# Kernel tuning notes

Measured on AMD Instinct MI355X. Metric: run time of the kernel, lower is better.

## Reference

```python
import jax, jax.numpy as jnp
import numpy as np
import math

N_EMBD = 1024
N_HEAD = 16
BLOCK_SIZE = 2048
B, T = 2, 2048


def setup_inputs() -> dict:
    key = jax.random.key(0)
    ks = jax.random.split(key, 12)
    s = 0.02
    C = N_EMBD
    return {
        "x": jax.random.normal(ks[0], (B, T, C), dtype=jnp.float32),
        # LayerNorm 1
        "ln1_w": jnp.ones((C,), jnp.float32),
        "ln1_b": jnp.zeros((C,), jnp.float32),
        # attention: weights stored [in, out]
        "attn_w": jax.random.normal(ks[1], (C, 3 * C), dtype=jnp.float32) * s,
        "attn_b": jnp.zeros((3 * C,), jnp.float32),
        "proj_w": jax.random.normal(ks[2], (C, C), dtype=jnp.float32) * s,
        "proj_b": jnp.zeros((C,), jnp.float32),
        # LayerNorm 2
        "ln2_w": jnp.ones((C,), jnp.float32),
        "ln2_b": jnp.zeros((C,), jnp.float32),
        # MLP
        "fc_w": jax.random.normal(ks[3], (C, 4 * C), dtype=jnp.float32) * s,
        "fc_b": jnp.zeros((4 * C,), jnp.float32),
        "mlp_proj_w": jax.random.normal(ks[4], (4 * C, C), dtype=jnp.float32) * s,
        "mlp_proj_b": jnp.zeros((C,), jnp.float32),
    }


def _layernorm(x, w, b, eps=1e-5):
    mu = jnp.mean(x, axis=-1, keepdims=True)
    var = jnp.mean(jnp.square(x - mu), axis=-1, keepdims=True)
    return (x - mu) * jax.lax.rsqrt(var + eps) * w + b


def _attention(x, attn_w, attn_b, proj_w, proj_b):
    Bn, Tn, C = x.shape
    hs = C // N_HEAD
    qkv = x @ attn_w + attn_b                      # [B,T,3C]
    q, k, v = jnp.split(qkv, 3, axis=-1)
    # [B,H,T,hs]
    q = q.reshape(Bn, Tn, N_HEAD, hs).transpose(0, 2, 1, 3)
    k = k.reshape(Bn, Tn, N_HEAD, hs).transpose(0, 2, 1, 3)
    v = v.reshape(Bn, Tn, N_HEAD, hs).transpose(0, 2, 1, 3)
    att = jnp.einsum('bhqd,bhkd->bhqk', q, k) / math.sqrt(hs)  # [B,H,T,T]
    mask = jnp.tril(jnp.ones((Tn, Tn), dtype=bool))
    att = jnp.where(mask, att, -jnp.inf)
    att = jax.nn.softmax(att, axis=-1)
    y = jnp.einsum('bhqk,bhkd->bhqd', att, v)      # [B,H,T,hs]
    y = y.transpose(0, 2, 1, 3).reshape(Bn, Tn, C)
    return y @ proj_w + proj_b


def reference(x, ln1_w, ln1_b, attn_w, attn_b, proj_w, proj_b,
              ln2_w, ln2_b, fc_w, fc_b, mlp_proj_w, mlp_proj_b):
    x = x + _attention(_layernorm(x, ln1_w, ln1_b), attn_w, attn_b, proj_w, proj_b)
    h = _layernorm(x, ln2_w, ln2_b)
    h = jax.nn.gelu(h @ fc_w + fc_b, approximate=False)  # torch nn.GELU default = exact erf
    return x + (h @ mlp_proj_w + mlp_proj_b)
```

## Files before the change

kernel.cpp:

```cpp
#include <hip/hip_runtime.h>
#include <math.h>

typedef short s8x __attribute__((ext_vector_type(8)));
typedef float f32x4 __attribute__((ext_vector_type(4)));
typedef int   i32x2 __attribute__((ext_vector_type(2)));

__device__ __forceinline__ float bf2f(short u) {
    return __uint_as_float(((unsigned int)(unsigned short)u) << 16);
}
__device__ __forceinline__ short f2bf(float f) {
    unsigned int x = __float_as_uint(f);
    unsigned int r = (x + 0x7FFFu + ((x >> 16) & 1u)) >> 16;
    return (short)(unsigned short)r;
}

__device__ __forceinline__ void gl2lds16(const short* g, const short* l) {
    __builtin_amdgcn_global_load_lds(
        (const __attribute__((address_space(1))) void*)(unsigned long long)g,
        (__attribute__((address_space(3))) void*)(unsigned int)(unsigned long long)l,
        16, 0, 0);
}

__device__ __forceinline__ void ln_row(const float* __restrict__ xin,
                                       const float* __restrict__ w,
                                       const float* __restrict__ bb,
                                       short* __restrict__ out, int row, int lane) {
    const float4* xr = (const float4*)(xin + (long)row * 1024);
    float4 v[4];
    float s1 = 0.f, s2 = 0.f;
#pragma unroll
    for (int i = 0; i < 4; ++i) {
        v[i] = xr[lane + i * 64];
        s1 += v[i].x + v[i].y + v[i].z + v[i].w;
        s2 += v[i].x*v[i].x + v[i].y*v[i].y + v[i].z*v[i].z + v[i].w*v[i].w;
    }
#pragma unroll
    for (int off = 32; off > 0; off >>= 1) {
        s1 += __shfl_xor(s1, off, 64);
        s2 += __shfl_xor(s2, off, 64);
    }
    const float mu = s1 * (1.0f / 1024.0f);
    float var = s2 * (1.0f / 1024.0f) - mu * mu;
    var = fmaxf(var, 0.0f);
    const float rs = rsqrtf(var + 1e-5f);
    short4* orow = (short4*)(out + (long)row * 1024);
#pragma unroll
    for (int i = 0; i < 4; ++i) {
        const int ci = (lane + i * 64) * 4;
        const float4 wv = *(const float4*)(w + ci);
        const float4 bv = *(const float4*)(bb + ci);
        short4 o;
        o.x = f2bf((v[i].x - mu) * rs * wv.x + bv.x);
        o.y = f2bf((v[i].y - mu) * rs * wv.y + bv.y);
        o.z = f2bf((v[i].z - mu) * rs * wv.z + bv.z);
        o.w = f2bf((v[i].w - mu) * rs * wv.w + bv.w);
        orow[lane + i * 64] = o;
    }
}

__global__ __launch_bounds__(256) void ln_k(const float* __restrict__ xin,
                                            const float* __restrict__ w,
                                            const float* __restrict__ bb,
                                            short* __restrict__ out) {
    ln_row(xin, w, bb, out, blockIdx.x * 4 + (threadIdx.x >> 6), threadIdx.x & 63);
}

__global__ __launch_bounds__(256) void pre_k(
        const float* __restrict__ w0, const float* __restrict__ w1,
        const float* __restrict__ w2, const float* __restrict__ w3,
        short* __restrict__ o0, short* __restrict__ o1,
        short* __restrict__ o2, short* __restrict__ o3,
        const float* __restrict__ x, const float* __restrict__ ln1w,
        const float* __restrict__ ln1b, short* __restrict__ xln) {
    int bid = blockIdx.x;
    if (bid >= 12288) {
        ln_row(x, ln1w, ln1b, xln, (bid - 12288) * 4 + (threadIdx.x >> 6), threadIdx.x & 63);
        return;
    }
    const float* in; short* out; int K, N, nx;
    if (bid < 3072)      { in = w0; out = o0; K = 1024; N = 3072; nx = 96; }
    else if (bid < 4096) { bid -= 3072; in = w1; out = o1; K = 1024; N = 1024; nx = 32; }
    else if (bid < 8192) { bid -= 4096; in = w2; out = o2; K = 1024; N = 4096; nx = 128; }
    else                 { bid -= 8192; in = w3; out = o3; K = 4096; N = 1024; nx = 32; }
    const int n0 = (bid % nx) * 32, k0 = (bid / nx) * 32;
    __shared__ float tile[32][33];
    const int tx = threadIdx.x & 31, ty = threadIdx.x >> 5;
#pragma unroll
    for (int i = 0; i < 4; ++i) {
        const int k = ty + i * 8;
        tile[k][tx] = in[(long)(k0 + k) * N + n0 + tx];
    }
    __syncthreads();
#pragma unroll
    for (int i = 0; i < 4; ++i) {
        const int n = ty + i * 8;
        out[(long)(n0 + n) * K + k0 + tx] = f2bf(tile[tx][n]);
    }
}

template <int EPI, typename OutT>
__device__ __forceinline__ void epi_store(OutT* out, const float* resid, long oidx, float v) {
    if constexpr (EPI == 0) {
        out[oidx] = f2bf(v);
    } else if constexpr (EPI == 1) {
        const float u = v * (0.79788456080f + 0.03567740814f * v * v);
        v = v / (1.0f + __expf(-2.0f * u));
        out[oidx] = f2bf(v);
    } else {
        v += resid[oidx];
        out[oidx] = v;
    }
}

template <int EPI, typename OutT>
__global__ __launch_bounds__(256) void gemm_k(const short* __restrict__ A,
                                              const short* __restrict__ Bt,
                                              const float* __restrict__ bias,
                                              const float* __restrict__ resid,
                                              OutT* __restrict__ out,
                                              int M, int N, int K) {
    __shared__ __align__(16) short sA[2][128 * 32];
    __shared__ __align__(16) short sB[2][128 * 32];
    const int tid = threadIdx.x;
    const int lane = tid & 63, wave = tid >> 6;
    const int wr = (wave >> 1) * 64, wc = (wave & 1) * 64;
    const int lrow = lane & 15, quad = lane >> 4;
    const int bm = blockIdx.y * 128, bn = blockIdx.x * 128;
    const short* Ap = A + (long)(bm + (tid >> 2)) * K + (tid & 3) * 8;
    const short* Bp = Bt + (long)(bn + (tid >> 2)) * K + (tid & 3) * 8;
    const long rowstep = (long)64 * K;

    auto stage = [&](int p, int k0) {
        gl2lds16(Ap + k0,           sA[p] + tid * 8);
        gl2lds16(Ap + rowstep + k0, sA[p] + 2048 + tid * 8);
        gl2lds16(Bp + k0,           sB[p] + tid * 8);
        gl2lds16(Bp + rowstep + k0, sB[p] + 2048 + tid * 8);
    };

    f32x4 acc[4][4] = {};
    stage(0, 0);
    const int S = K >> 5;
    for (int s = 0; s < S; ++s) {
        const int p = s & 1;
        __syncthreads();
        if (s + 1 < S) stage(p ^ 1, (s + 1) << 5);
        const short* pA = sA[p];
        const short* pB = sB[p];
        s8x af[4], bfr[4];
#pragma unroll
        for (int i = 0; i < 4; ++i) af[i]  = *(const s8x*)(pA + (wr + i*16 + lrow) * 32 + quad * 8);
#pragma unroll
        for (int j = 0; j < 4; ++j) bfr[j] = *(const s8x*)(pB + (wc + j*16 + lrow) * 32 + quad * 8);
#pragma unroll
        for (int i = 0; i < 4; ++i)
#pragma unroll
            for (int j = 0; j < 4; ++j)
                acc[i][j] = __builtin_amdgcn_mfma_f32_16x16x32_bf16(af[i], bfr[j], acc[i][j], 0, 0, 0);
    }
#pragma unroll
    for (int i = 0; i < 4; ++i) {
#pragma unroll
        for (int j = 0; j < 4; ++j) {
#pragma unroll
            for (int r = 0; r < 4; ++r) {
                const int row = bm + wr + i*16 + quad*4 + r;
                const int col = bn + wc + j*16 + lrow;
                epi_store<EPI>(out, resid, (long)row * N + col, acc[i][j][r] + bias[col]);
            }
        }
    }
}

template <int EPI, typename OutT>
__global__ __launch_bounds__(256) void gemm128x64_k(const short* __restrict__ A,
                                                    const short* __restrict__ Bt,
                                                    const float* __restrict__ bias,
                                                    const float* __restrict__ resid,
                                                    OutT* __restrict__ out,
                                                    int M, int N, int K) {
    __shared__ __align__(16) short sA[2][2][128 * 32];
    __shared__ __align__(16) short sB[2][2][64 * 32];
    const int tid = threadIdx.x;
    const int lane = tid & 63, wave = tid >> 6;
    const int wr = (wave >> 1) * 64, wc = (wave & 1) * 32;
    const int lrow = lane & 15, quad = lane >> 4;
    const int bm = blockIdx.y * 128, bn = blockIdx.x * 64;
    const short* Ap = A + (long)(bm + (tid >> 2)) * K + (tid & 3) * 8;
    const short* Bp = Bt + (long)(bn + (tid >> 2)) * K + (tid & 3) * 8;
    const long rowstep = (long)64 * K;

    auto stage = [&](int p, int k0) {
#pragma unroll
        for (int hp = 0; hp < 2; ++hp) {
            gl2lds16(Ap + k0 + hp * 32,           sA[p][hp] + tid * 8);
            gl2lds16(Ap + rowstep + k0 + hp * 32, sA[p][hp] + 2048 + tid * 8);
            gl2lds16(Bp + k0 + hp * 32,           sB[p][hp] + tid * 8);
        }
    };

    f32x4 acc[4][2] = {};
    stage(0, 0);
    const int S = K >> 6;
    for (int s = 0; s < S; ++s) {
        const int p = s & 1;
        __syncthreads();
        if (s + 1 < S) stage(p ^ 1, (s + 1) << 6);
#pragma unroll
        for (int hp = 0; hp < 2; ++hp) {
            s8x af[4], bfr[2];
#pragma unroll
            for (int i = 0; i < 4; ++i) af[i]  = *(const s8x*)(sA[p][hp] + (wr + i*16 + lrow) * 32 + quad * 8);
#pragma unroll
            for (int j = 0; j < 2; ++j) bfr[j] = *(const s8x*)(sB[p][hp] + (wc + j*16 + lrow) * 32 + quad * 8);
#pragma unroll
            for (int i = 0; i < 4; ++i)
#pragma unroll
                for (int j = 0; j < 2; ++j)
                    acc[i][j] = __builtin_amdgcn_mfma_f32_16x16x32_bf16(af[i], bfr[j], acc[i][j], 0, 0, 0);
        }
    }
#pragma unroll
    for (int i = 0; i < 4; ++i) {
#pragma unroll
        for (int j = 0; j < 2; ++j) {
#pragma unroll
            for (int r = 0; r < 4; ++r) {
                const int row = bm + wr + i*16 + quad*4 + r;
                const int col = bn + wc + j*16 + lrow;
                epi_store<EPI>(out, resid, (long)row * N + col, acc[i][j][r] + bias[col]);
            }
        }
    }
}

#define ATT_CS (0.125f * 1.4426950408889634f)
#define ATT_C0 (14.426950408889634f)

#define TR16(dst, off) \
    asm volatile("ds_read_b64_tr_b16 %0, %1 offset:" off : "=v"(dst) : "v"(tva))

__global__ __launch_bounds__(256) void attn_k(const short* __restrict__ qkv,
                                              short* __restrict__ y) {
    const int bx = blockIdx.x;
    const int b = blockIdx.y >> 4, h = blockIdx.y & 15;
    const int qtA = bx, qtB = 31 - bx;
    const int tid = threadIdx.x, lane = tid & 63, wave = tid >> 6;
    const int lrow = lane & 15, quad = lane >> 4;
    const long base = (long)b * 2048 * 3072;

    __shared__ __align__(16) short sK[2][64 * 64];
    __shared__ __align__(16) short sV[2][4096];

    s8x qfA0, qfA1, qfB0, qfB1;
    {
        const short* qpA = qkv + base + (long)(qtA * 64 + wave * 16 + lrow) * 3072 + h * 64 + quad * 8;
        qfA0 = *(const s8x*)qpA; qfA1 = *(const s8x*)(qpA + 32);
        const short* qpB = qkv + base + (long)(qtB * 64 + wave * 16 + lrow) * 3072 + h * 64 + quad * 8;
        qfB0 = *(const s8x*)qpB; qfB1 = *(const s8x*)(qpB + 32);
    }
    f32x4 oA[4], oB[4];
    float lA = 0.f, lB = 0.f;
#pragma unroll
    for (int d = 0; d < 4; ++d) { oA[d] = f32x4{0.f,0.f,0.f,0.f}; oB[d] = f32x4{0.f,0.f,0.f,0.f}; }

    const int srow = tid >> 3, sg = tid & 7;
    const int sw0 = ((srow & 7) ^ (srow >> 3)) & 7;
    const int sw1 = (((srow + 32) & 7) ^ ((srow + 32) >> 3)) & 7;
    const short* kbase = qkv + base + 1024 + h * 64;
    auto issueK = [&](int p, int k0) {
        gl2lds16(kbase + (long)(k0 + srow) * 3072      + (sg ^ sw0) * 8, sK[p] + tid * 8);
        gl2lds16(kbase + (long)(k0 + srow + 32) * 3072 + (sg ^ sw1) * 8, sK[p] + 2048 + tid * 8);
    };

    const int vslot   = (tid >> 3) & 7;
    const int vkbl    = 2 * (vslot & 3) + (vslot >> 2);
    const int vklocal = vkbl * 4 + ((tid >> 1) & 3);
    const short* vsrc = qkv + base + 2048 + h * 64
                      + (long)vklocal * 3072 + wave * 16 + 8 * (tid & 1);
    auto issueV = [&](int p, int k0) {
        gl2lds16(vsrc + (long)k0 * 3072,        sV[p] + tid * 8);
        gl2lds16(vsrc + (long)(k0 + 32) * 3072, sV[p] + 2048 + tid * 8);
    };
    const unsigned trb = (unsigned)(unsigned long long)(&sV[0][0]) + (unsigned)lane * 8u;

    auto tile_step = [&](const s8x& qf0, const s8x& qf1, const s8x* kf0, const s8x* kf1,
                         const s8x (*vfr)[4], f32x4* o, float& lsum, int qt, int kt, int k0) {
        f32x4 s[4];
#pragma unroll
        for (int ct = 0; ct < 4; ++ct) {
            f32x4 t = f32x4{0.f, 0.f, 0.f, 0.f};
            t = __builtin_amdgcn_mfma_f32_16x16x32_bf16(kf0[ct], qf0, t, 0, 0, 0);
            t = __builtin_amdgcn_mfma_f32_16x16x32_bf16(kf1[ct], qf1, t, 0, 0, 0);
            s[ct] = t;
        }
        const int qrow = qt * 64 + wave * 16 + lrow;
        float pv[4][4];
        if (kt == qt) {
#pragma unroll
            for (int ct = 0; ct < 4; ++ct)
#pragma unroll
                for (int r = 0; r < 4; ++r) {
                    const int key = k0 + ct * 16 + quad * 4 + r;
                    const float pp = exp2f(fmaf(s[ct][r], ATT_CS, -ATT_C0));
                    const float pt = __uint_as_float(__float_as_uint(pp) & 0xFFFF0000u);
                    pv[ct][r] = (key > qrow) ? 0.f : pt;
                }
        } else {
#pragma unroll
            for (int ct = 0; ct < 4; ++ct)
#pragma unroll
                for (int r = 0; r < 4; ++r) {
                    const float pp = exp2f(fmaf(s[ct][r], ATT_CS, -ATT_C0));
                    pv[ct][r] = __uint_as_float(__float_as_uint(pp) & 0xFFFF0000u);
                }
        }
#pragma unroll
        for (int ct = 0; ct < 4; ++ct)
            lsum += (pv[ct][0] + pv[ct][1]) + (pv[ct][2] + pv[ct][3]);

        unsigned int w2[4][2];
#pragma unroll
        for (int ct = 0; ct < 4; ++ct)
#pragma unroll
            for (int p2 = 0; p2 < 2; ++p2)
                w2[ct][p2] = __builtin_amdgcn_perm(__float_as_uint(pv[ct][2 * p2 + 1]),
                                                   __float_as_uint(pv[ct][2 * p2]), 0x07060302u);
        s8x pa[2];
#pragma unroll
        for (int ks = 0; ks < 2; ++ks) {
            auto rAC = __builtin_amdgcn_permlane32_swap((int)w2[2 * ks][0], (int)w2[2 * ks + 1][0], false, false);
            auto rBD = __builtin_amdgcn_permlane32_swap((int)w2[2 * ks][1], (int)w2[2 * ks + 1][1], false, false);
            auto mAC = __builtin_amdgcn_permlane16_swap(rAC[0], rAC[1], false, false);
            auto mBD = __builtin_amdgcn_permlane16_swap(rBD[0], rBD[1], false, false);
            int4 f;
            f.x = mAC[0]; f.y = mBD[0]; f.z = mAC[1]; f.w = mBD[1];
            pa[ks] = *(const s8x*)&f;
        }
#pragma unroll
        for (int ks = 0; ks < 2; ++ks)
#pragma unroll
            for (int dt = 0; dt < 4; ++dt)
                o[dt] = __builtin_amdgcn_mfma_f32_16x16x32_bf16(pa[ks], vfr[ks][dt], o[dt], 0, 0, 0);
    };

    issueK(0, 0);
    issueV(0, 0);
    for (int kt = 0; kt <= qtB; ++kt) {
        const int p = kt & 1, k0 = kt * 64;
        __syncthreads();
        if (kt < qtB) { issueK(p ^ 1, k0 + 64); issueV(p ^ 1, k0 + 64); }

        s8x kf0[4], kf1[4];
#pragma unroll
        for (int ct = 0; ct < 4; ++ct) {
            const int row = ct * 16 + lrow;
            const int swr = ((row & 7) ^ (row >> 3)) & 7;
            kf0[ct] = *(const s8x*)(sK[p] + row * 64 + ((quad ^ swr) * 8));
            kf1[ct] = *(const s8x*)(sK[p] + row * 64 + (((4 + quad) ^ swr) * 8));
        }

        const unsigned tva = trb + (unsigned)(p << 13);
        i32x2 tr[16];
        TR16(tr[0],  "0");    TR16(tr[1],  "512");
        TR16(tr[2],  "1024"); TR16(tr[3],  "1536");
        TR16(tr[4],  "2048"); TR16(tr[5],  "2560");
        TR16(tr[6],  "3072"); TR16(tr[7],  "3584");
        TR16(tr[8],  "4096"); TR16(tr[9],  "4608");
        TR16(tr[10], "5120"); TR16(tr[11], "5632");
        TR16(tr[12], "6144"); TR16(tr[13], "6656");
        TR16(tr[14], "7168"); TR16(tr[15], "7680");
        asm volatile("s_waitcnt lgkmcnt(0)" ::: "memory");
        __builtin_amdgcn_sched_barrier(0);
        s8x vfr[2][4];
#pragma unroll
        for (int ks = 0; ks < 2; ++ks)
#pragma unroll
            for (int dt = 0; dt < 4; ++dt) {
                const int i2 = ks * 8 + dt * 2;
                int4 f;
                f.x = tr[i2][0]; f.y = tr[i2][1];
                f.z = tr[i2 + 1][0]; f.w = tr[i2 + 1][1];
                vfr[ks][dt] = *(const s8x*)&f;
            }

        if (kt <= qtA) tile_step(qfA0, qfA1, kf0, kf1, vfr, oA, lA, qtA, kt, k0);
        tile_step(qfB0, qfB1, kf0, kf1, vfr, oB, lB, qtB, kt, k0);
    }

    lA += __shfl_xor(lA, 16, 64); lA += __shfl_xor(lA, 32, 64);
    lB += __shfl_xor(lB, 16, 64); lB += __shfl_xor(lB, 32, 64);
    float rA[4], rB[4];
#pragma unroll
    for (int r = 0; r < 4; ++r) {
        rA[r] = 1.0f / __shfl(lA, quad * 4 + r, 64);
        rB[r] = 1.0f / __shfl(lB, quad * 4 + r, 64);
    }
#pragma unroll
    for (int dt = 0; dt < 4; ++dt) {
#pragma unroll
        for (int r = 0; r < 4; ++r) {
            const int qA = qtA * 64 + wave * 16 + quad * 4 + r;
            const int qB = qtB * 64 + wave * 16 + quad * 4 + r;
            y[((long)b * 2048 + qA) * 1024 + h * 64 + dt * 16 + lrow] = f2bf(oA[dt][r] * rA[r]);
            y[((long)b * 2048 + qB) * 1024 + h * 64 + dt * 16 + lrow] = f2bf(oB[dt][r] * rB[r]);
        }
    }
}

extern "C" void kernel_launch(void* const* d_in, const int* in_sizes, int n_in,
                              void* d_out, int out_size, void* d_ws, size_t ws_size,
                              hipStream_t stream) {
    const float* x      = (const float*)d_in[0];
    const float* ln1_w  = (const float*)d_in[1];
    const float* ln1_b  = (const float*)d_in[2];
    const float* attn_w = (const float*)d_in[3];
    const float* attn_b = (const float*)d_in[4];
    const float* proj_w = (const float*)d_in[5];
    const float* proj_b = (const float*)d_in[6];
    const float* ln2_w  = (const float*)d_in[7];
    const float* ln2_b  = (const float*)d_in[8];
    const float* fc_w   = (const float*)d_in[9];
    const float* fc_b   = (const float*)d_in[10];
    const float* mlp_w  = (const float*)d_in[11];
    const float* mlp_b  = (const float*)d_in[12];

    char* ws = (char*)d_ws;
    short* attn_wt = (short*)(ws + 0);
    short* proj_wt = (short*)(ws + 6291456L);
    short* fc_wt   = (short*)(ws + 8388608L);
    short* mlp_wt  = (short*)(ws + 16777216L);
    short* slotA   = (short*)(ws + 25165824L);
    short* slotB   = (short*)(ws + 33554432L);

    short* xln  = slotA;
    short* yb   = slotA;
    short* hb   = slotA;
    short* qkvb = slotB;
    short* hh   = slotB;
    float* x1   = (float*)d_out;
    float* outp = (float*)d_out;

    pre_k<<<13312, 256, 0, stream>>>(attn_w, proj_w, fc_w, mlp_w,
                                     attn_wt, proj_wt, fc_wt, mlp_wt,
                                     x, ln1_w, ln1_b, xln);

    gemm_k<0, short><<<dim3(24, 32), 256, 0, stream>>>(xln, attn_wt, attn_b, nullptr, qkvb, 4096, 3072, 1024);
    attn_k<<<dim3(16, 32), 256, 0, stream>>>(qkvb, yb);
    gemm128x64_k<2, float><<<dim3(16, 32), 256, 0, stream>>>(yb, proj_wt, proj_b, x, x1, 4096, 1024, 1024);
    ln_k<<<1024, 256, 0, stream>>>(x1, ln2_w, ln2_b, hb);
    gemm_k<1, short><<<dim3(32, 32), 256, 0, stream>>>(hb, fc_wt, fc_b, nullptr, hh, 4096, 4096, 1024);
    gemm128x64_k<3, float><<<dim3(16, 32), 256, 0, stream>>>(hh, mlp_wt, mlp_b, x1, outp, 4096, 1024, 4096);
}
```

Before: 331.1 us.

## Triple-buffer LDS staging in GEMM and attention with explicit vmcnt waits

Moves the GEMM and attention kernels from double to triple LDS buffering. Global-to-LDS loads are issued two tiles ahead, and the full __syncthreads is replaced by an explicit vmcnt wait plus a raw s_barrier. The goal is to hide global load latency behind more MFMA work. It costs 50% more LDS per block, which may lower occupancy, and relies on correct vmcnt counting.

```diff
diff --git a/kernel.cpp b/kernel.cpp
--- a/kernel.cpp
+++ b/kernel.cpp
@@ -20,6 +20,13 @@
         (__attribute__((address_space(3))) void*)(unsigned int)(unsigned long long)l,
         16, 0, 0);
 }
+
+__device__ __forceinline__ void block_sync() {
+    asm volatile("" ::: "memory");
+    __builtin_amdgcn_s_barrier();
+    asm volatile("" ::: "memory");
+}
+#define WAITV(n) asm volatile("s_waitcnt vmcnt(" #n ")" ::: "memory")
 
 __device__ __forceinline__ void ln_row(const float* __restrict__ xin,
                                        const float* __restrict__ w,
@@ -119,8 +126,8 @@
                                               const float* __restrict__ resid,
                                               OutT* __restrict__ out,
                                               int M, int N, int K) {
-    __shared__ __align__(16) short sA[2][128 * 32];
-    __shared__ __align__(16) short sB[2][128 * 32];
+    __shared__ __align__(16) short sA[3][128 * 32];
+    __shared__ __align__(16) short sB[3][128 * 32];
     const int tid = threadIdx.x;
     const int lane = tid & 63, wave = tid >> 6;
     const int wr = (wave >> 1) * 64, wc = (wave & 1) * 64;
@@ -130,22 +137,24 @@
     const short* Bp = Bt + (long)(bn + (tid >> 2)) * K + (tid & 3) * 8;
     const long rowstep = (long)64 * K;
 
-    auto stage = [&](int p, int k0) {
-        gl2lds16(Ap + k0,           sA[p] + tid * 8);
-        gl2lds16(Ap + rowstep + k0, sA[p] + 2048 + tid * 8);
-        gl2lds16(Bp + k0,           sB[p] + tid * 8);
-        gl2lds16(Bp + rowstep + k0, sB[p] + 2048 + tid * 8);
+    auto stage = [&](int q, int k0) {
+        gl2lds16(Ap + k0,           sA[q] + tid * 8);
+        gl2lds16(Ap + rowstep + k0, sA[q] + 2048 + tid * 8);
+        gl2lds16(Bp + k0,           sB[q] + tid * 8);
+        gl2lds16(Bp + rowstep + k0, sB[q] + 2048 + tid * 8);
     };
 
     f32x4 acc[4][4] = {};
+    const int S = K >> 5;
     stage(0, 0);
-    const int S = K >> 5;
+    stage(1, 32);
+    int cur = 0, nx2 = 2;
     for (int s = 0; s < S; ++s) {
-        const int p = s & 1;
-        __syncthreads();
-        if (s + 1 < S) stage(p ^ 1, (s + 1) << 5);
-        const short* pA = sA[p];
-        const short* pB = sB[p];
+        if (s + 1 < S) { WAITV(4); } else { WAITV(0); }
+        block_sync();
+        if (s + 2 < S) stage(nx2, (s + 2) << 5);
+        const short* pA = sA[cur];
+        const short* pB = sB[cur];
         s8x af[4], bfr[4];
 #pragma unroll
         for (int i = 0; i < 4; ++i) af[i]  = *(const s8x*)(pA + (wr + i*16 + lrow) * 32 + quad * 8);
@@ -156,6 +165,8 @@
 #pragma unroll
             for (int j = 0; j < 4; ++j)
                 acc[i][j] = __builtin_amdgcn_mfma_f32_16x16x32_bf16(af[i], bfr[j], acc[i][j], 0, 0, 0);
+        cur = (cur == 2) ? 0 : cur + 1;
+        nx2 = (nx2 == 2) ? 0 : nx2 + 1;
     }
 #pragma unroll
     for (int i = 0; i < 4; ++i) {
@@ -248,8 +259,8 @@
     const int lrow = lane & 15, quad = lane >> 4;
     const long base = (long)b * 2048 * 3072;
 
-    __shared__ __align__(16) short sK[2][64 * 64];
-    __shared__ __align__(16) short sV[2][4096];
+    __shared__ __align__(16) short sK[3][64 * 64];
+    __shared__ __align__(16) short sV[3][4096];
 
     s8x qfA0, qfA1, qfB0, qfB1;
     {
@@ -267,9 +278,9 @@
     const int sw0 = ((srow & 7) ^ (srow >> 3)) & 7;
     const int sw1 = (((srow + 32) & 7) ^ ((srow + 32) >> 3)) & 7;
     const short* kbase = qkv + base + 1024 + h * 64;
-    auto issueK = [&](int p, int k0) {
-        gl2lds16(kbase + (long)(k0 + srow) * 3072      + (sg ^ sw0) * 8, sK[p] + tid * 8);
-        gl2lds16(kbase + (long)(k0 + srow + 32) * 3072 + (sg ^ sw1) * 8, sK[p] + 2048 + tid * 8);
+    auto issueK = [&](int q, int k0) {
+        gl2lds16(kbase + (long)(k0 + srow) * 3072      + (sg ^ sw0) * 8, sK[q] + tid * 8);
+        gl2lds16(kbase + (long)(k0 + srow + 32) * 3072 + (sg ^ sw1) * 8, sK[q] + 2048 + tid * 8);
     };
 
     const int vslot   = (tid >> 3) & 7;
@@ -277,9 +288,9 @@
     const int vklocal = vkbl * 4 + ((tid >> 1) & 3);
     const short* vsrc = qkv + base + 2048 + h * 64
                       + (long)vklocal * 3072 + wave * 16 + 8 * (tid & 1);
-    auto issueV = [&](int p, int k0) {
-        gl2lds16(vsrc + (long)k0 * 3072,        sV[p] + tid * 8);
-        gl2lds16(vsrc + (long)(k0 + 32) * 3072, sV[p] + 2048 + tid * 8);
+    auto issueV = [&](int q, int k0) {
+        gl2lds16(vsrc + (long)k0 * 3072,        sV[q] + tid * 8);
+        gl2lds16(vsrc + (long)(k0 + 32) * 3072, sV[q] + 2048 + tid * 8);
     };
     const unsigned trb = (unsigned)(unsigned long long)(&sV[0][0]) + (unsigned)lane * 8u;
 
@@ -343,23 +354,25 @@
                 o[dt] = __builtin_amdgcn_mfma_f32_16x16x32_bf16(pa[ks], vfr[ks][dt], o[dt], 0, 0, 0);
     };
 
-    issueK(0, 0);
-    issueV(0, 0);
+    issueK(0, 0);   issueV(0, 0);
+    issueK(1, 64);  issueV(1, 64);
+    int cur = 0, nx2 = 2;
     for (int kt = 0; kt <= qtB; ++kt) {
-        const int p = kt & 1, k0 = kt * 64;
-        __syncthreads();
-        if (kt < qtB) { issueK(p ^ 1, k0 + 64); issueV(p ^ 1, k0 + 64); }
+        const int k0 = kt * 64;
+        if (kt < qtB) { WAITV(4); } else { WAITV(0); }
+        block_sync();
+        if (kt + 2 <= qtB) { issueK(nx2, k0 + 128); issueV(nx2, k0 + 128); }
 
         s8x kf0[4], kf1[4];
 #pragma unroll
         for (int ct = 0; ct < 4; ++ct) {
             const int row = ct * 16 + lrow;
             const int swr = ((row & 7) ^ (row >> 3)) & 7;
-            kf0[ct] = *(const s8x*)(sK[p] + row * 64 + ((quad ^ swr) * 8));
-            kf1[ct] = *(const s8x*)(sK[p] + row * 64 + (((4 + quad) ^ swr) * 8));
-        }
-
-        const unsigned tva = trb + (unsigned)(p << 13);
+            kf0[ct] = *(const s8x*)(sK[cur] + row * 64 + ((quad ^ swr) * 8));
+            kf1[ct] = *(const s8x*)(sK[cur] + row * 64 + (((4 + quad) ^ swr) * 8));
+        }
+
+        const unsigned tva = trb + (unsigned)(cur << 13);
         i32x2 tr[16];
         TR16(tr[0],  "0");    TR16(tr[1],  "512");
         TR16(tr[2],  "1024"); TR16(tr[3],  "1536");
@@ -385,6 +398,9 @@
 
         if (kt <= qtA) tile_step(qfA0, qfA1, kf0, kf1, vfr, oA, lA, qtA, kt, k0);
         tile_step(qfB0, qfB1, kf0, kf1, vfr, oB, lB, qtB, kt, k0);
+
+        cur = (cur == 2) ? 0 : cur + 1;
+        nx2 = (nx2 == 2) ? 0 : nx2 + 1;
     }
 
     lA += __shfl_xor(lA, 16, 64); lA += __shfl_xor(lA, 32, 64);
```

Result: no change. 337.0 us (+1.8%).
